# Kernel optimization log

Hardware: AMD Instinct MI355X
Metric: run time of the kernel (lower is better)

Reference implementation:

```python
import jax, jax.numpy as jnp
import numpy as np

KEEP_RATIO = 0.5  # init kwarg keep_ratio
B, S, D = 8, 8192, 1024


def setup_inputs() -> dict:
    key = jax.random.key(0)
    k1, k2, k3 = jax.random.split(key, 3)
    hidden_states = jax.random.normal(k1, (B, S, D), dtype=jnp.float32)
    active_mask = jax.random.bernoulli(k2, 0.8, (B, S))
    scorer_w = jax.random.normal(k3, (D,), dtype=jnp.float32) / np.sqrt(D)
    scorer_b = jnp.zeros((1,), dtype=jnp.float32)
    return {"hidden_states": hidden_states, "active_mask": active_mask,
            "scorer_w": scorer_w, "scorer_b": scorer_b}


def reference(hidden_states, active_mask, scorer_w, scorer_b):
    # scores = Linear(d_model -> 1).squeeze(-1)  -> [B, S]
    scores = jnp.einsum('bsd,d->bs', hidden_states, scorer_w) + scorer_b[0]
    # masked_fill(~active, -inf)
    masked = jnp.where(active_mask, scores, -jnp.inf)
    # per-row variable k = max(1, ceil(n_active * keep_ratio))
    n_active = jnp.sum(active_mask, axis=-1)                      # [B] int
    k = jnp.maximum(1, jnp.ceil(n_active.astype(jnp.float32) * KEEP_RATIO)).astype(jnp.int32)
    # rank of each token within its row by descending masked score;
    # inactive tokens (-inf) sort last, so rank < k selects the top-k active tokens
    order = jnp.argsort(-masked, axis=-1)      # [B, S] indices, best first
    ranks = jnp.argsort(order, axis=-1)        # [B, S] rank per position
    keep_mask = (ranks < k[:, None]) & active_mask
    return keep_mask
```

## Files before the change

### kernel.cpp

```cpp
#include <hip/hip_runtime.h>
#include <math.h>

#define BB 8
#define SS 8192
#define DD 1024
#define NTOK (BB * SS)
#define NWAVES 8192
#define TOK_PER_WAVE (NTOK / NWAVES)

__device__ __forceinline__ float dot4(float4 a, float4 b) {
    return a.x * b.x + a.y * b.y + a.z * b.z + a.w * b.w;
}

__global__ __launch_bounds__(256) void score_kernel(
    const float* __restrict__ hs, const int* __restrict__ mask,
    const float* __restrict__ w, const float* __restrict__ bias,
    float* __restrict__ scores)
{
    const int gw   = blockIdx.x * 4 + (threadIdx.x >> 6);
    const int lane = threadIdx.x & 63;

    const float4* wp = (const float4*)w;
    const float4 w0 = wp[lane];
    const float4 w1 = wp[lane + 64];
    const float4 w2 = wp[lane + 128];
    const float4 w3 = wp[lane + 192];
    const float b = bias[0];

#pragma unroll
    for (int t = 0; t < TOK_PER_WAVE; t += 2) {
        const int tokA = t * NWAVES + gw;
        const int tokB = (t + 1) * NWAVES + gw;
        const float4* hA = (const float4*)(hs + (size_t)tokA * DD);
        const float4* hB = (const float4*)(hs + (size_t)tokB * DD);

        float4 a0 = hA[lane];       float4 a1 = hA[lane + 64];
        float4 a2 = hA[lane + 128]; float4 a3 = hA[lane + 192];
        float4 c0 = hB[lane];       float4 c1 = hB[lane + 64];
        float4 c2 = hB[lane + 128]; float4 c3 = hB[lane + 192];

        float sA = dot4(a0, w0) + dot4(a1, w1) + dot4(a2, w2) + dot4(a3, w3);
        float sB = dot4(c0, w0) + dot4(c1, w1) + dot4(c2, w2) + dot4(c3, w3);

#pragma unroll
        for (int off = 32; off > 0; off >>= 1) {
            sA += __shfl_down(sA, off, 64);
            sB += __shfl_down(sB, off, 64);
        }
        if (lane == 0) {
            scores[tokA] = (mask[tokA] != 0) ? (sA + b) : -INFINITY;
            scores[tokB] = (mask[tokB] != 0) ? (sB + b) : -INFINITY;
        }
    }
}

__global__ __launch_bounds__(1024) void select_kernel(
    const int* __restrict__ mask, float* __restrict__ buf)
{
    __shared__ unsigned int keys[SS];
    __shared__ unsigned int hist[256];
    __shared__ unsigned int wsum[16];
    __shared__ unsigned int n_active_sh;
    __shared__ unsigned int sel_bin, sel_knew;

    const int row = blockIdx.x;
    const int tid = threadIdx.x;
    const float* srow = buf + row * SS;
    const int* mrow = mask + row * SS;

    if (tid == 0) n_active_sh = 0;
    __syncthreads();

    unsigned int mycnt = 0;
    for (int i = tid; i < SS; i += 1024) {
        unsigned int u = __float_as_uint(srow[i]);
        keys[i] = (u & 0x80000000u) ? ~u : (u | 0x80000000u);
        if (mrow[i] != 0) mycnt++;
    }
    atomicAdd(&n_active_sh, mycnt);
    __syncthreads();

    const unsigned int n_active = n_active_sh;
    unsigned int k = (n_active + 1u) >> 1;
    if (k < 1u) k = 1u;

    unsigned int prefix = 0, prefmask = 0;
    for (int round = 0; round < 4; ++round) {
        const int shift = 24 - 8 * round;
        if (tid < 256) hist[tid] = 0;
        __syncthreads();
        for (int i = tid; i < SS; i += 1024) {
            unsigned int key = keys[i];
            if ((key & prefmask) == prefix)
                atomicAdd(&hist[(key >> shift) & 0xFFu], 1u);
        }
        __syncthreads();
        if (tid < 64) {
            const int lane = tid;
            unsigned int h0 = hist[4 * lane];
            unsigned int h1 = hist[4 * lane + 1];
            unsigned int h2 = hist[4 * lane + 2];
            unsigned int h3 = hist[4 * lane + 3];
            unsigned int local = h0 + h1 + h2 + h3;
            unsigned int suf = local;
#pragma unroll
            for (int off = 1; off < 64; off <<= 1) {
                unsigned int v = (unsigned int)__shfl_down((int)suf, off, 64);
                if (lane + off < 64) suf += v;
            }
            unsigned int above = suf - local;
            unsigned int s3 = h3 + above;
            unsigned int s2 = h2 + s3;
            unsigned int s1 = h1 + s2;
            unsigned int s0 = h0 + s1;
            if (s3 >= k && above < k) { sel_bin = 4u*lane + 3u; sel_knew = k - above; }
            if (s2 >= k && s3    < k) { sel_bin = 4u*lane + 2u; sel_knew = k - s3; }
            if (s1 >= k && s2    < k) { sel_bin = 4u*lane + 1u; sel_knew = k - s2; }
            if (s0 >= k && s1    < k) { sel_bin = 4u*lane;      sel_knew = k - s1; }
        }
        __syncthreads();
        prefix |= sel_bin << shift;
        prefmask |= 0xFFu << shift;
        k = sel_knew;
        __syncthreads();
    }

    const unsigned int thr = prefix;
    const unsigned int k_rem = k;

    const int base = tid * 8;
    unsigned int cnt = 0;
#pragma unroll
    for (int j = 0; j < 8; ++j) cnt += (keys[base + j] == thr) ? 1u : 0u;

    const int lane = tid & 63, wv = tid >> 6;
    unsigned int inc = cnt;
#pragma unroll
    for (int off = 1; off < 64; off <<= 1) {
        unsigned int n = (unsigned int)__shfl_up((int)inc, off, 64);
        if (lane >= off) inc += n;
    }
    if (lane == 63) wsum[wv] = inc;
    __syncthreads();
    if (tid == 0) {
        unsigned int acc = 0;
        for (int i = 0; i < 16; ++i) { unsigned int t = wsum[i]; wsum[i] = acc; acc += t; }
    }
    __syncthreads();
    unsigned int r = wsum[wv] + inc - cnt;

    int* orow = (int*)(buf + row * SS);
#pragma unroll
    for (int j = 0; j < 8; ++j) {
        const int i = base + j;
        const unsigned int key = keys[i];
        bool keep;
        if (key > thr) keep = true;
        else if (key == thr) { keep = (r < k_rem); r++; }
        else keep = false;
        keep = keep && (mrow[i] != 0);
        orow[i] = keep ? 1 : 0;
    }
}

extern "C" void kernel_launch(void* const* d_in, const int* in_sizes, int n_in,
                              void* d_out, int out_size, void* d_ws, size_t ws_size,
                              hipStream_t stream) {
    const float* hs   = (const float*)d_in[0];
    const int* msk    = (const int*)d_in[1];
    const float* w    = (const float*)d_in[2];
    const float* bias = (const float*)d_in[3];

    float* buf = (float*)d_out;

    score_kernel<<<NWAVES / 4, 256, 0, stream>>>(hs, msk, w, bias, buf);
    select_kernel<<<BB, 1024, 0, stream>>>(msk, buf);
}
```

Measured before the change: 374.3 us.

## Fuse scoring and top-k selection into one kernel with a grid-wide completion counter

Merges the score and select kernels into a single launch. Every block scores its tokens, then increments a global counter. The first eight blocks spin until all blocks are done and then run the per-row radix select. This removes one kernel launch and the gap between the two kernels, at the cost of a memset, 1024-thread blocks that reserve 32KB of shared memory each (which can lower occupancy of the bandwidth-bound scoring phase), and a spin-wait that relies on all 512 blocks being co-resident or scheduled in a way that avoids deadlock.

```diff
diff --git a/kernel.cpp b/kernel.cpp
--- a/kernel.cpp
+++ b/kernel.cpp
@@ -7,18 +7,27 @@
 #define NTOK (BB * SS)
 #define NWAVES 8192
 #define TOK_PER_WAVE (NTOK / NWAVES)
+#define WPB 16
+#define GRID (NWAVES / WPB)
 
 __device__ __forceinline__ float dot4(float4 a, float4 b) {
     return a.x * b.x + a.y * b.y + a.z * b.z + a.w * b.w;
 }
 
-__global__ __launch_bounds__(256) void score_kernel(
+__global__ __launch_bounds__(1024) void fused_kernel(
     const float* __restrict__ hs, const int* __restrict__ mask,
     const float* __restrict__ w, const float* __restrict__ bias,
-    float* __restrict__ scores)
+    float* __restrict__ buf, unsigned int* __restrict__ done)
 {
-    const int gw   = blockIdx.x * 4 + (threadIdx.x >> 6);
-    const int lane = threadIdx.x & 63;
+    __shared__ unsigned int keys[SS];
+    __shared__ unsigned int hist[256];
+    __shared__ unsigned int wsum[WPB];
+    __shared__ unsigned int n_active_sh, sel_bin, sel_knew;
+
+    const int tid  = threadIdx.x;
+    const int widx = tid >> 6;
+    const int lane = tid & 63;
+    const int gw   = blockIdx.x * WPB + widx;
 
     const float4* wp = (const float4*)w;
     const float4 w0 = wp[lane];
@@ -48,28 +57,28 @@
             sB += __shfl_down(sB, off, 64);
         }
         if (lane == 0) {
-            scores[tokA] = (mask[tokA] != 0) ? (sA + b) : -INFINITY;
-            scores[tokB] = (mask[tokB] != 0) ? (sB + b) : -INFINITY;
+            buf[tokA] = (mask[tokA] != 0) ? (sA + b) : -INFINITY;
+            buf[tokB] = (mask[tokB] != 0) ? (sB + b) : -INFINITY;
         }
     }
-}
 
-__global__ __launch_bounds__(1024) void select_kernel(
-    const int* __restrict__ mask, float* __restrict__ buf)
-{
-    __shared__ unsigned int keys[SS];
-    __shared__ unsigned int hist[256];
-    __shared__ unsigned int wsum[16];
-    __shared__ unsigned int n_active_sh;
-    __shared__ unsigned int sel_bin, sel_knew;
+    __threadfence();
+    __syncthreads();
+    if (tid == 0) atomicAdd(done, 1u);
+
+    if (blockIdx.x >= BB) return;
 
     const int row = blockIdx.x;
-    const int tid = threadIdx.x;
+    if (tid == 0) {
+        while (atomicAdd(done, 0u) < (unsigned int)GRID)
+            __builtin_amdgcn_s_sleep(2);
+        n_active_sh = 0;
+    }
+    __syncthreads();
+    __threadfence();
+
     const float* srow = buf + row * SS;
     const int* mrow = mask + row * SS;
-
-    if (tid == 0) n_active_sh = 0;
-    __syncthreads();
 
     unsigned int mycnt = 0;
     for (int i = tid; i < SS; i += 1024) {
@@ -96,27 +105,27 @@
         }
         __syncthreads();
         if (tid < 64) {
-            const int lane = tid;
-            unsigned int h0 = hist[4 * lane];
-            unsigned int h1 = hist[4 * lane + 1];
-            unsigned int h2 = hist[4 * lane + 2];
-            unsigned int h3 = hist[4 * lane + 3];
+            const int ln = tid;
+            unsigned int h0 = hist[4 * ln];
+            unsigned int h1 = hist[4 * ln + 1];
+            unsigned int h2 = hist[4 * ln + 2];
+            unsigned int h3 = hist[4 * ln + 3];
             unsigned int local = h0 + h1 + h2 + h3;
             unsigned int suf = local;
 #pragma unroll
             for (int off = 1; off < 64; off <<= 1) {
                 unsigned int v = (unsigned int)__shfl_down((int)suf, off, 64);
-                if (lane + off < 64) suf += v;
+                if (ln + off < 64) suf += v;
             }
             unsigned int above = suf - local;
             unsigned int s3 = h3 + above;
             unsigned int s2 = h2 + s3;
             unsigned int s1 = h1 + s2;
             unsigned int s0 = h0 + s1;
-            if (s3 >= k && above < k) { sel_bin = 4u*lane + 3u; sel_knew = k - above; }
-            if (s2 >= k && s3    < k) { sel_bin = 4u*lane + 2u; sel_knew = k - s3; }
-            if (s1 >= k && s2    < k) { sel_bin = 4u*lane + 1u; sel_knew = k - s2; }
-            if (s0 >= k && s1    < k) { sel_bin = 4u*lane;      sel_knew = k - s1; }
+            if (s3 >= k && above < k) { sel_bin = 4u*ln + 3u; sel_knew = k - above; }
+            if (s2 >= k && s3    < k) { sel_bin = 4u*ln + 2u; sel_knew = k - s3; }
+            if (s1 >= k && s2    < k) { sel_bin = 4u*ln + 1u; sel_knew = k - s2; }
+            if (s0 >= k && s1    < k) { sel_bin = 4u*ln;      sel_knew = k - s1; }
         }
         __syncthreads();
         prefix |= sel_bin << shift;
@@ -133,21 +142,20 @@
 #pragma unroll
     for (int j = 0; j < 8; ++j) cnt += (keys[base + j] == thr) ? 1u : 0u;
 
-    const int lane = tid & 63, wv = tid >> 6;
     unsigned int inc = cnt;
 #pragma unroll
     for (int off = 1; off < 64; off <<= 1) {
         unsigned int n = (unsigned int)__shfl_up((int)inc, off, 64);
         if (lane >= off) inc += n;
     }
-    if (lane == 63) wsum[wv] = inc;
+    if (lane == 63) wsum[widx] = inc;
     __syncthreads();
     if (tid == 0) {
         unsigned int acc = 0;
-        for (int i = 0; i < 16; ++i) { unsigned int t = wsum[i]; wsum[i] = acc; acc += t; }
+        for (int i = 0; i < WPB; ++i) { unsigned int t = wsum[i]; wsum[i] = acc; acc += t; }
     }
     __syncthreads();
-    unsigned int r = wsum[wv] + inc - cnt;
+    unsigned int r = wsum[widx] + inc - cnt;
 
     int* orow = (int*)(buf + row * SS);
 #pragma unroll
@@ -172,7 +180,8 @@
     const float* bias = (const float*)d_in[3];
 
     float* buf = (float*)d_out;
+    unsigned int* done = (unsigned int*)d_ws;
 
-    score_kernel<<<NWAVES / 4, 256, 0, stream>>>(hs, msk, w, bias, buf);
-    select_kernel<<<BB, 1024, 0, stream>>>(msk, buf);
+    hipMemsetAsync(d_ws, 0, 64, stream);
+    fused_kernel<<<GRID, 1024, 0, stream>>>(hs, msk, w, bias, buf, done);
 }
```

Result: slower. 672.1 us (+79.6%).
